# Optimization experiments

Measured on AMD Instinct MI355X. Metric: run time of the kernel, lower is better.

## Reference

```python
import jax, jax.numpy as jnp
import numpy as np

# FP4 (e2m1) representable magnitudes: {0, 0.5, 1, 1.5, 2, 3, 4, 6}
_FP4_GRID = np.array([0.0, 0.5, 1.0, 1.5, 2.0, 3.0, 4.0, 6.0], dtype=np.float32)
_FP4_MIDS = (_FP4_GRID[1:] + _FP4_GRID[:-1]) / 2.0  # decision boundaries


def quant_fp4(x):
    """Per-tensor symmetric quantize-dequantize to FP4 e2m1 grid."""
    grid = jnp.asarray(_FP4_GRID, dtype=x.dtype)
    mids = jnp.asarray(_FP4_MIDS, dtype=x.dtype)
    scale = jnp.maximum(jnp.max(jnp.abs(x)) / 6.0, jnp.asarray(1e-12, x.dtype))
    xs = jnp.abs(x) / scale
    idx = jnp.searchsorted(mids, xs)  # nearest-grid-point index
    return jnp.sign(x) * grid[idx] * scale


def fp4_linear(x, w, b):
    # fake-quantized matmul: dequant(FP4(x)) @ dequant(FP4(w)) + b
    return jnp.matmul(quant_fp4(x), quant_fp4(w)) + b


def setup_inputs() -> dict:
    key = jax.random.key(0)
    k1, k2, k3 = jax.random.split(key, 3)
    B, D_IN, D_H, D_OUT = 4096, 4096, 16384, 4096
    x = jax.random.normal(k1, (B, D_IN), dtype=jnp.float32)
    w1 = jax.random.normal(k2, (D_IN, D_H), dtype=jnp.float32)
    b1 = jnp.zeros((D_H,), dtype=jnp.float32)
    w2 = jax.random.normal(k3, (D_H, D_OUT), dtype=jnp.float32)
    b2 = jnp.zeros((D_OUT,), dtype=jnp.float32)
    return {"x": x, "w1": w1, "b1": b1, "w2": w2, "b2": b2}


def reference(x, w1, b1, w2, b2):
    h = jax.nn.relu(fp4_linear(x, w1, b1))
    return fp4_linear(h, w2, b2)
```

## Files before the change

### kernel.cpp

```cpp
#include <hip/hip_runtime.h>
#include <hip/hip_bf16.h>


typedef float f32x4 __attribute__((ext_vector_type(4)));
typedef int   i32x4 __attribute__((ext_vector_type(4)));
typedef int   i32x8 __attribute__((ext_vector_type(8)));

#define AS1 __attribute__((address_space(1)))
#define AS3 __attribute__((address_space(3)))

__device__ __forceinline__ float scale_from_amax_bits(unsigned bits) {
    return fmaxf(__uint_as_float(bits) / 6.0f, 1e-12f);
}

__device__ __forceinline__ unsigned q4(float v, float inv_scale) {
    float xs = fabsf(v) * inv_scale;
    unsigned idx = 0;
    idx += (xs > 0.25f);
    idx += (xs > 0.75f);
    idx += (xs > 1.25f);
    idx += (xs > 1.75f);
    idx += (xs > 2.5f);
    idx += (xs > 3.5f);
    idx += (xs > 5.0f);
    return idx | ((v < 0.0f) ? 8u : 0u);
}

__global__ void zero4_kernel(unsigned* p) {
    if (threadIdx.x < 4) p[threadIdx.x] = 0u;
}

__global__ void sentinel_kernel(float* out, long long n) {
    long long i = (long long)blockIdx.x * blockDim.x + threadIdx.x;
    long long stride = (long long)gridDim.x * blockDim.x;
    for (; i < n; i += stride) out[i] = 1e30f;
}

__global__ void absmax3_kernel(const float* __restrict__ in0, long long n0,
                               const float* __restrict__ in1, long long n1,
                               const float* __restrict__ in2, long long n2,
                               unsigned* __restrict__ out) {
    const float* in;
    long long n;
    unsigned* o;
    long long nb, b = blockIdx.x;
    if (b < 512)       { in = in0; n = n0; o = out + 0; b -= 0;    nb = 512;  }
    else if (b < 2560) { in = in1; n = n1; o = out + 1; b -= 512;  nb = 2048; }
    else               { in = in2; n = n2; o = out + 3; b -= 2560; nb = 2048; }

    long long i = (b * blockDim.x + threadIdx.x) * 4;
    long long stride = nb * blockDim.x * 4;
    float m = 0.0f;
    for (; i < n; i += stride) {
        float4 v = *(const float4*)&in[i];
        m = fmaxf(m, fmaxf(fmaxf(fabsf(v.x), fabsf(v.y)),
                           fmaxf(fabsf(v.z), fabsf(v.w))));
    }
    #pragma unroll
    for (int off = 32; off > 0; off >>= 1)
        m = fmaxf(m, __shfl_xor(m, off));
    __shared__ float smax[4];
    int lane = threadIdx.x & 63, w = threadIdx.x >> 6;
    if (lane == 0) smax[w] = m;
    __syncthreads();
    if (threadIdx.x == 0) {
        m = fmaxf(fmaxf(smax[0], smax[1]), fmaxf(smax[2], smax[3]));
        atomicMax(o, __float_as_uint(m));
    }
}

__global__ void quant_pack_kernel(const float* __restrict__ in, long long n,
                                  const unsigned* __restrict__ amax,
                                  unsigned* __restrict__ out) {
    float inv = 1.0f / scale_from_amax_bits(*amax);
    long long i = ((long long)blockIdx.x * blockDim.x + threadIdx.x) * 8;
    long long stride = (long long)gridDim.x * blockDim.x * 8;
    for (; i < n; i += stride) {
        float4 a = *(const float4*)&in[i];
        float4 b = *(const float4*)&in[i + 4];
        unsigned u = q4(a.x, inv)        | (q4(a.y, inv) << 4)
                   | (q4(a.z, inv) << 8) | (q4(a.w, inv) << 12)
                   | (q4(b.x, inv) << 16)| (q4(b.y, inv) << 20)
                   | (q4(b.z, inv) << 24)| (q4(b.w, inv) << 28);
        out[i >> 3] = u;
    }
}

__global__ void quant_transpose_pack_kernel(const float* __restrict__ in, int R, int C,
                                            const unsigned* __restrict__ amax,
                                            unsigned char* __restrict__ out) {
    __shared__ float tile[64][65];
    float inv = 1.0f / scale_from_amax_bits(*amax);
    int t = threadIdx.x;
    int CT = C >> 6;
    int tc = blockIdx.x % CT;
    int tr = blockIdx.x / CT;
    int r0 = t >> 4;
    int c0 = (t & 15) * 4;
    #pragma unroll
    for (int it = 0; it < 4; ++it) {
        int r = r0 + it * 16;
        float4 v = *(const float4*)&in[(size_t)(tr * 64 + r) * C + tc * 64 + c0];
        tile[r][c0 + 0] = v.x;
        tile[r][c0 + 1] = v.y;
        tile[r][c0 + 2] = v.z;
        tile[r][c0 + 3] = v.w;
    }
    __syncthreads();
    int c = t >> 2;
    int rch = (t & 3) * 16;
    unsigned u0 = 0, u1 = 0;
    #pragma unroll
    for (int j = 0; j < 8; ++j) u0 |= q4(tile[rch + j][c], inv) << (4 * j);
    #pragma unroll
    for (int j = 0; j < 8; ++j) u1 |= q4(tile[rch + 8 + j][c], inv) << (4 * j);
    uint2 o; o.x = u0; o.y = u1;
    *(uint2*)&out[(size_t)(tc * 64 + c) * (R >> 1) + (size_t)(tr * 32) + (rch >> 1)] = o;
}

template <int RELU, int FUSE_AMAX>
__global__ __launch_bounds__(256, 2)
void gemm_fp4_dbuf(const unsigned char* __restrict__ Ap,
                   const unsigned char* __restrict__ Bp,
                   float* __restrict__ C, const float* __restrict__ bias,
                   const unsigned* __restrict__ amaxA,
                   const unsigned* __restrict__ amaxB,
                   unsigned* __restrict__ amaxOut,
                   int M, int N, int K) {
    __shared__ alignas(16) unsigned char As[2][128 * 128];
    __shared__ alignas(16) unsigned char Bs[2][128 * 128];
    __shared__ float smax[4];

    int nwg = gridDim.x;
    int cpx = nwg >> 3;
    int wg = (blockIdx.x & 7) * cpx + (blockIdx.x >> 3);
    int MT = M >> 7;
    int tm = wg % MT;
    int tn = wg / MT;

    int tid = threadIdx.x;
    int lane = tid & 63;
    int wid = tid >> 6;
    int wr = wid >> 1, wc = wid & 1;

    size_t Kb = (size_t)(K >> 1);

    int cs = ((lane & 7) ^ ((lane >> 3) & 7)) << 4;
    int srow = wid * 32 + (lane >> 3);
    const unsigned char* Abase = Ap + (size_t)(tm * 128 + srow) * Kb + cs;
    const unsigned char* Bbase = Bp + (size_t)(tn * 128 + srow) * Kb + cs;
    char* AsB = (char*)As;
    char* BsB = (char*)Bs;
    int ldsOff = wid * 4096;

#define STAGE(d, kt)                                                          \
    do {                                                                      \
        _Pragma("unroll")                                                     \
        for (int i_ = 0; i_ < 4; ++i_) {                                      \
            __builtin_amdgcn_global_load_lds(                                 \
                (const AS1 void*)(Abase + (size_t)(kt) * 128 +                \
                                  (size_t)(i_ * 8) * Kb),                     \
                (AS3 void*)(AsB + ((d) << 14) + ldsOff + i_ * 1024),          \
                16, 0, 0);                                                    \
            __builtin_amdgcn_global_load_lds(                                 \
                (const AS1 void*)(Bbase + (size_t)(kt) * 128 +                \
                                  (size_t)(i_ * 8) * Kb),                     \
                (AS3 void*)(BsB + ((d) << 14) + ldsOff + i_ * 1024),          \
                16, 0, 0);                                                    \
        }                                                                     \
    } while (0)

    f32x4 acc[4][4] = {};
    int rrA = wr * 64 + (lane & 15);
    int rrB = wc * 64 + (lane & 15);

    int KT = K >> 8;

    STAGE(0, 0);
    __syncthreads();

    for (int t = 0; t < KT; ++t) {
        int d = t & 1;
        if (t + 1 < KT) STAGE(d ^ 1, t + 1);
        __builtin_amdgcn_sched_barrier(0);

        const char* Aq = AsB + (d << 14);
        const char* Bq = BsB + (d << 14);
        #pragma unroll
        for (int ks = 0; ks < 2; ++ks) {
            int slotOff = ((ks * 4 + (lane >> 4)) ^ (lane & 7)) << 4;
            i32x8 a8[4], b8[4];
            #pragma unroll
            for (int mi = 0; mi < 4; ++mi) {
                i32x4 v = *(const i32x4*)(Aq + (rrA + mi * 16) * 128 + slotOff);
                a8[mi] = i32x8{v[0], v[1], v[2], v[3], 0, 0, 0, 0};
            }
            #pragma unroll
            for (int ni = 0; ni < 4; ++ni) {
                i32x4 v = *(const i32x4*)(Bq + (rrB + ni * 16) * 128 + slotOff);
                b8[ni] = i32x8{v[0], v[1], v[2], v[3], 0, 0, 0, 0};
            }
            #pragma unroll
            for (int mi = 0; mi < 4; ++mi)
                #pragma unroll
                for (int ni = 0; ni < 4; ++ni)
                    acc[mi][ni] = __builtin_amdgcn_mfma_scale_f32_16x16x128_f8f6f4(
                        a8[mi], b8[ni], acc[mi][ni],
                        4, 4,
                        0, 0x7f7f7f7f,
                        0, 0x7f7f7f7f);
        }
        __syncthreads();
    }
#undef STAGE

    float sa = scale_from_amax_bits(*amaxA);
    float sb = scale_from_amax_bits(*amaxB);
    float s = sa * sb;
    float vmax = 0.0f;
    int rowBase = tm * 128 + wr * 64 + (lane >> 4) * 4;
    int colBase = tn * 128 + wc * 64 + (lane & 15);
    #pragma unroll
    for (int mi = 0; mi < 4; ++mi) {
        #pragma unroll
        for (int ni = 0; ni < 4; ++ni) {
            int col = colBase + ni * 16;
            float bv = bias[col];
            int row = rowBase + mi * 16;
            #pragma unroll
            for (int r = 0; r < 4; ++r) {
                float v = acc[mi][ni][r] * s + bv;
                if (RELU) v = fmaxf(v, 0.0f);
                if (FUSE_AMAX) vmax = fmaxf(vmax, fabsf(v));
                C[(size_t)(row + r) * N + col] = v;
            }
        }
    }
    if (FUSE_AMAX) {
        #pragma unroll
        for (int off = 32; off > 0; off >>= 1)
            vmax = fmaxf(vmax, __shfl_xor(vmax, off));
        if (lane == 0) smax[wid] = vmax;
        __syncthreads();
        if (tid == 0) {
            vmax = fmaxf(fmaxf(smax[0], smax[1]), fmaxf(smax[2], smax[3]));
            atomicMax(amaxOut, __float_as_uint(vmax));
        }
    }
}

extern "C" void kernel_launch(void* const* d_in, const int* in_sizes, int n_in,
                              void* d_out, int out_size, void* d_ws, size_t ws_size,
                              hipStream_t stream) {
    const float* x  = (const float*)d_in[0];
    const float* w1 = (const float*)d_in[1];
    const float* b1 = (const float*)d_in[2];
    const float* w2 = (const float*)d_in[3];
    const float* b2 = (const float*)d_in[4];
    float* out = (float*)d_out;

    const int B = 4096, DIN = 4096, DH = 16384, DOUT = 4096;

    const size_t off_amax = 0;
    const size_t off_Xq   = 256;
    const size_t off_W    = off_Xq + (size_t)B * DIN / 2;
    const size_t off_h    = off_W + (size_t)DIN * DH / 2;
    const size_t off_Hq   = off_h + (size_t)B * DH * 4;
    const size_t needed   = off_Hq + (size_t)B * DH / 2;

    if (ws_size < needed) {
        sentinel_kernel<<<2048, 256, 0, stream>>>(out, (long long)out_size);
        return;
    }

    char* ws = (char*)d_ws;
    unsigned* amax = (unsigned*)(ws + off_amax);
    unsigned char* Xq = (unsigned char*)(ws + off_Xq);
    unsigned char* Wq = (unsigned char*)(ws + off_W);
    float*         h  = (float*)(ws + off_h);
    unsigned char* Hq = (unsigned char*)(ws + off_Hq);

    zero4_kernel<<<1, 64, 0, stream>>>(amax);

    absmax3_kernel<<<4608, 256, 0, stream>>>(x, (long long)B * DIN,
                                             w1, (long long)DIN * DH,
                                             w2, (long long)DH * DOUT, amax);

    quant_pack_kernel<<<2048, 256, 0, stream>>>(x, (long long)B * DIN, amax + 0,
                                                (unsigned*)Xq);
    quant_transpose_pack_kernel<<<(DIN / 64) * (DH / 64), 256, 0, stream>>>(
        w1, DIN, DH, amax + 1, Wq);

    gemm_fp4_dbuf<1, 1><<<(B / 128) * (DH / 128), 256, 0, stream>>>(
        Xq, Wq, h, b1, amax + 0, amax + 1, amax + 2, B, DH, DIN);

    quant_pack_kernel<<<2048, 256, 0, stream>>>(h, (long long)B * DH, amax + 2,
                                                (unsigned*)Hq);
    quant_transpose_pack_kernel<<<(DH / 64) * (DOUT / 64), 256, 0, stream>>>(
        w2, DH, DOUT, amax + 3, Wq);

    gemm_fp4_dbuf<0, 0><<<(B / 128) * (DOUT / 128), 256, 0, stream>>>(
        Hq, Wq, out, b2, amax + 2, amax + 3, nullptr, B, DOUT, DH);
}
```

Measured before the change: 753.6 us.

## Halve GEMM K-step to 128 and use 128x64 tiles for first FP4 GEMM

Both FP4 GEMMs now stage 64-byte (128-element) K slices per iteration instead of 256, halving shared memory per stage and changing the XOR swizzle to match. The first GEMM gets a new variant with 128x64 output tiles, twice the blocks, and launch bounds raised to 4 waves-per-EU targets. The goal is higher occupancy and better latency hiding. The cost is more loop iterations and barriers per K, and less data reuse per tile in the first GEMM.

```diff
diff --git a/kernel.cpp b/kernel.cpp
--- a/kernel.cpp
+++ b/kernel.cpp
@@ -118,54 +118,59 @@
     *(uint2*)&out[(size_t)(tc * 64 + c) * (R >> 1) + (size_t)(tr * 32) + (rch >> 1)] = o;
 }
 
+__device__ __forceinline__ f32x4 mm16(i32x4 a, i32x4 b, f32x4 c) {
+    i32x8 a8 = {a[0], a[1], a[2], a[3], 0, 0, 0, 0};
+    i32x8 b8 = {b[0], b[1], b[2], b[3], 0, 0, 0, 0};
+    return __builtin_amdgcn_mfma_scale_f32_16x16x128_f8f6f4(
+        a8, b8, c, 4, 4,
+        0, 0x7f7f7f7f,
+        0, 0x7f7f7f7f);
+}
+
 template <int RELU, int FUSE_AMAX>
 __global__ __launch_bounds__(256, 2)
-void gemm_fp4_dbuf(const unsigned char* __restrict__ Ap,
-                   const unsigned char* __restrict__ Bp,
-                   float* __restrict__ C, const float* __restrict__ bias,
-                   const unsigned* __restrict__ amaxA,
-                   const unsigned* __restrict__ amaxB,
-                   unsigned* __restrict__ amaxOut,
-                   int M, int N, int K) {
-    __shared__ alignas(16) unsigned char As[2][128 * 128];
-    __shared__ alignas(16) unsigned char Bs[2][128 * 128];
+void gemm_fp4_v1(const unsigned char* __restrict__ Ap,
+                 const unsigned char* __restrict__ Bp,
+                 float* __restrict__ C, const float* __restrict__ bias,
+                 const unsigned* __restrict__ amaxA,
+                 const unsigned* __restrict__ amaxB,
+                 unsigned* __restrict__ amaxOut,
+                 int M, int N, int K) {
+    __shared__ alignas(16) unsigned char As[2][128 * 64];
+    __shared__ alignas(16) unsigned char Bs[2][128 * 64];
     __shared__ float smax[4];
 
-    int nwg = gridDim.x;
-    int cpx = nwg >> 3;
+    int nwg = gridDim.x, cpx = nwg >> 3;
     int wg = (blockIdx.x & 7) * cpx + (blockIdx.x >> 3);
     int MT = M >> 7;
-    int tm = wg % MT;
-    int tn = wg / MT;
-
-    int tid = threadIdx.x;
-    int lane = tid & 63;
-    int wid = tid >> 6;
+    int tm = wg % MT, tn = wg / MT;
+
+    int tid = threadIdx.x, lane = tid & 63, wid = tid >> 6;
     int wr = wid >> 1, wc = wid & 1;
 
     size_t Kb = (size_t)(K >> 1);
 
-    int cs = ((lane & 7) ^ ((lane >> 3) & 7)) << 4;
-    int srow = wid * 32 + (lane >> 3);
-    const unsigned char* Abase = Ap + (size_t)(tm * 128 + srow) * Kb + cs;
-    const unsigned char* Bbase = Bp + (size_t)(tn * 128 + srow) * Kb + cs;
+    int csw = ((tid & 3) ^ ((tid >> 3) & 3)) << 4;
+    int srow = tid >> 2;
+    const unsigned char* Abase = Ap + (size_t)(tm * 128 + srow) * Kb + csw;
+    const unsigned char* Bbase = Bp + (size_t)(tn * 128 + srow) * Kb + csw;
     char* AsB = (char*)As;
     char* BsB = (char*)Bs;
-    int ldsOff = wid * 4096;
-
-#define STAGE(d, kt)                                                          \
+    int dstOff = wid << 10;
+
+#define STAGE1(d, kt)                                                         \
     do {                                                                      \
         _Pragma("unroll")                                                     \
-        for (int i_ = 0; i_ < 4; ++i_) {                                      \
+        for (int i_ = 0; i_ < 2; ++i_) {                                      \
             __builtin_amdgcn_global_load_lds(                                 \
-                (const AS1 void*)(Abase + (size_t)(kt) * 128 +                \
-                                  (size_t)(i_ * 8) * Kb),                     \
-                (AS3 void*)(AsB + ((d) << 14) + ldsOff + i_ * 1024),          \
+                (const AS1 void*)(Abase + (size_t)(kt) * 64 +                 \
+                                  (size_t)(i_ * 64) * Kb),                    \
+                (AS3 void*)(AsB + ((d) << 13) + (i_ << 12) + dstOff),         \
                 16, 0, 0);                                                    \
             __builtin_amdgcn_global_load_lds(                                 \
-                (const AS1 void*)(Bbase + (size_t)(kt) * 128 +                \
-                                  (size_t)(i_ * 8) * Kb),                     \
-                (AS3 void*)(BsB + ((d) << 14) + ldsOff + i_ * 1024),          \
+                (const AS1 void*)(Bbase + (size_t)(kt) * 64 +                 \
+                                  (size_t)(i_ * 64) * Kb),                    \
+                (AS3 void*)(BsB + ((d) << 13) + (i_ << 12) + dstOff),         \
                 16, 0, 0);                                                    \
         }                                                                     \
     } while (0)
@@ -173,50 +178,37 @@
     f32x4 acc[4][4] = {};
     int rrA = wr * 64 + (lane & 15);
     int rrB = wc * 64 + (lane & 15);
-
-    int KT = K >> 8;
-
-    STAGE(0, 0);
+    int slotOff = (((lane >> 4) ^ ((lane >> 1) & 3)) << 4);
+
+    int KT = K >> 7;
+
+    STAGE1(0, 0);
     __syncthreads();
 
     for (int t = 0; t < KT; ++t) {
         int d = t & 1;
-        if (t + 1 < KT) STAGE(d ^ 1, t + 1);
+        if (t + 1 < KT) STAGE1(d ^ 1, t + 1);
         __builtin_amdgcn_sched_barrier(0);
 
-        const char* Aq = AsB + (d << 14);
-        const char* Bq = BsB + (d << 14);
-        #pragma unroll
-        for (int ks = 0; ks < 2; ++ks) {
-            int slotOff = ((ks * 4 + (lane >> 4)) ^ (lane & 7)) << 4;
-            i32x8 a8[4], b8[4];
+        const char* Aq = AsB + (d << 13);
+        const char* Bq = BsB + (d << 13);
+        i32x4 a[4], b[4];
+        #pragma unroll
+        for (int mi = 0; mi < 4; ++mi)
+            a[mi] = *(const i32x4*)(Aq + (rrA + mi * 16) * 64 + slotOff);
+        #pragma unroll
+        for (int ni = 0; ni < 4; ++ni)
+            b[ni] = *(const i32x4*)(Bq + (rrB + ni * 16) * 64 + slotOff);
+        #pragma unroll
+        for (int mi = 0; mi < 4; ++mi)
             #pragma unroll
-            for (int mi = 0; mi < 4; ++mi) {
-                i32x4 v = *(const i32x4*)(Aq + (rrA + mi * 16) * 128 + slotOff);
-                a8[mi] = i32x8{v[0], v[1], v[2], v[3], 0, 0, 0, 0};
-            }
-            #pragma unroll
-            for (int ni = 0; ni < 4; ++ni) {
-                i32x4 v = *(const i32x4*)(Bq + (rrB + ni * 16) * 128 + slotOff);
-                b8[ni] = i32x8{v[0], v[1], v[2], v[3], 0, 0, 0, 0};
-            }
-            #pragma unroll
-            for (int mi = 0; mi < 4; ++mi)
-                #pragma unroll
-                for (int ni = 0; ni < 4; ++ni)
-                    acc[mi][ni] = __builtin_amdgcn_mfma_scale_f32_16x16x128_f8f6f4(
-                        a8[mi], b8[ni], acc[mi][ni],
-                        4, 4,
-                        0, 0x7f7f7f7f,
-                        0, 0x7f7f7f7f);
-        }
+            for (int ni = 0; ni < 4; ++ni)
+                acc[mi][ni] = mm16(a[mi], b[ni], acc[mi][ni]);
         __syncthreads();
     }
-#undef STAGE
-
-    float sa = scale_from_amax_bits(*amaxA);
-    float sb = scale_from_amax_bits(*amaxB);
-    float s = sa * sb;
+#undef STAGE1
+
+    float s = scale_from_amax_bits(*amaxA) * scale_from_amax_bits(*amaxB);
     float vmax = 0.0f;
     int rowBase = tm * 128 + wr * 64 + (lane >> 4) * 4;
     int colBase = tn * 128 + wc * 64 + (lane & 15);
@@ -249,6 +241,118 @@
     }
 }
 
+template <int RELU, int FUSE_AMAX>
+__global__ __launch_bounds__(256, 4)
+void gemm_fp4_v2(const unsigned char* __restrict__ Ap,
+                 const unsigned char* __restrict__ Bp,
+                 float* __restrict__ C, const float* __restrict__ bias,
+                 const unsigned* __restrict__ amaxA,
+                 const unsigned* __restrict__ amaxB,
+                 unsigned* __restrict__ amaxOut,
+                 int M, int N, int K) {
+    __shared__ alignas(16) unsigned char As[2][128 * 64];
+    __shared__ alignas(16) unsigned char Bs[2][64 * 64];
+    __shared__ float smax[4];
+
+    int nwg = gridDim.x, cpx = nwg >> 3;
+    int wg = (blockIdx.x & 7) * cpx + (blockIdx.x >> 3);
+    int MT = M >> 7;
+    int tm = wg % MT, tn = wg / MT;
+
+    int tid = threadIdx.x, lane = tid & 63, wid = tid >> 6;
+    int wr = wid >> 1, wc = wid & 1;
+
+    size_t Kb = (size_t)(K >> 1);
+
+    int csw = ((tid & 3) ^ ((tid >> 3) & 3)) << 4;
+    int srow = tid >> 2;
+    const unsigned char* Abase = Ap + (size_t)(tm * 128 + srow) * Kb + csw;
+    const unsigned char* Bbase = Bp + (size_t)(tn * 64 + srow) * Kb + csw;
+    char* AsB = (char*)As;
+    char* BsB = (char*)Bs;
+    int dstOff = wid << 10;
+
+#define STAGE2(d, kt)                                                         \
+    do {                                                                      \
+        _Pragma("unroll")                                                     \
+        for (int i_ = 0; i_ < 2; ++i_) {                                      \
+            __builtin_amdgcn_global_load_lds(                                 \
+                (const AS1 void*)(Abase + (size_t)(kt) * 64 +                 \
+                                  (size_t)(i_ * 64) * Kb),                    \
+                (AS3 void*)(AsB + ((d) << 13) + (i_ << 12) + dstOff),         \
+                16, 0, 0);                                                    \
+        }                                                                     \
+        __builtin_amdgcn_global_load_lds(                                     \
+            (const AS1 void*)(Bbase + (size_t)(kt) * 64),                     \
+            (AS3 void*)(BsB + ((d) << 12) + dstOff), 16, 0, 0);               \
+    } while (0)
+
+    f32x4 acc[4][2] = {};
+    int rrA = wr * 64 + (lane & 15);
+    int rrB = wc * 32 + (lane & 15);
+    int slotOff = (((lane >> 4) ^ ((lane >> 1) & 3)) << 4);
+
+    int KT = K >> 7;
+
+    STAGE2(0, 0);
+    __syncthreads();
+
+    for (int t = 0; t < KT; ++t) {
+        int d = t & 1;
+        if (t + 1 < KT) STAGE2(d ^ 1, t + 1);
+        __builtin_amdgcn_sched_barrier(0);
+
+        const char* Aq = AsB + (d << 13);
+        const char* Bq = BsB + (d << 12);
+        i32x4 a[4], b[2];
+        #pragma unroll
+        for (int mi = 0; mi < 4; ++mi)
+            a[mi] = *(const i32x4*)(Aq + (rrA + mi * 16) * 64 + slotOff);
+        #pragma unroll
+        for (int ni = 0; ni < 2; ++ni)
+            b[ni] = *(const i32x4*)(Bq + (rrB + ni * 16) * 64 + slotOff);
+        #pragma unroll
+        for (int mi = 0; mi < 4; ++mi)
+            #pragma unroll
+            for (int ni = 0; ni < 2; ++ni)
+                acc[mi][ni] = mm16(a[mi], b[ni], acc[mi][ni]);
+        __syncthreads();
+    }
+#undef STAGE2
+
+    float s = scale_from_amax_bits(*amaxA) * scale_from_amax_bits(*amaxB);
+    float vmax = 0.0f;
+    int rowBase = tm * 128 + wr * 64 + (lane >> 4) * 4;
+    int colBase = tn * 64 + wc * 32 + (lane & 15);
+    #pragma unroll
+    for (int mi = 0; mi < 4; ++mi) {
+        #pragma unroll
+        for (int ni = 0; ni < 2; ++ni) {
+            int col = colBase + ni * 16;
+            float bv = bias[col];
+            int row = rowBase + mi * 16;
+            #pragma unroll
+            for (int r = 0; r < 4; ++r) {
+                float v = acc[mi][ni][r] * s + bv;
+                if (RELU) v = fmaxf(v, 0.0f);
+                if (FUSE_AMAX) vmax = fmaxf(vmax, fabsf(v));
+                C[(size_t)(row + r) * N + col] = v;
+            }
+        }
+    }
+    if (FUSE_AMAX) {
+        #pragma unroll
+        for (int off = 32; off > 0; off >>= 1)
+            vmax = fmaxf(vmax, __shfl_xor(vmax, off));
+        if (lane == 0) smax[wid] = vmax;
+        __syncthreads();
+        if (tid == 0) {
+            vmax = fmaxf(fmaxf(smax[0], smax[1]), fmaxf(smax[2], smax[3]));
+            atomicMax(amaxOut, __float_as_uint(vmax));
+        }
+    }
+}
+
 extern "C" void kernel_launch(void* const* d_in, const int* in_sizes, int n_in,
                               void* d_out, int out_size, void* d_ws, size_t ws_size,
                               hipStream_t stream) {
@@ -291,7 +395,7 @@
     quant_transpose_pack_kernel<<<(DIN / 64) * (DH / 64), 256, 0, stream>>>(
         w1, DIN, DH, amax + 1, Wq);
 
-    gemm_fp4_dbuf<1, 1><<<(B / 128) * (DH / 128), 256, 0, stream>>>(
+    gemm_fp4_v2<1, 1><<<(B / 128) * (DH / 64), 256, 0, stream>>>(
         Xq, Wq, h, b1, amax + 0, amax + 1, amax + 2, B, DH, DIN);
 
     quant_pack_kernel<<<2048, 256, 0, stream>>>(h, (long long)B * DH, amax + 2,
@@ -299,6 +403,6 @@
     quant_transpose_pack_kernel<<<(DH / 64) * (DOUT / 64), 256, 0, stream>>>(
         w2, DH, DOUT, amax + 3, Wq);
 
-    gemm_fp4_dbuf<0, 0><<<(B / 128) * (DOUT / 128), 256, 0, stream>>>(
+    gemm_fp4_v1<0, 0><<<(B / 128) * (DOUT / 128), 256, 0, stream>>>(
         Hq, Wq, out, b2, amax + 2, amax + 3, nullptr, B, DOUT, DH);
 }
```

Result: slower. 783.8 us (+4.0%).
